# Kernel tuning notes

Hardware: AMD Instinct MI355X
Metric: run time of the kernel (lower is better)

## Reference

```python
import jax, jax.numpy as jnp
import numpy as np

B, C, H, W = 8, 32, 512, 512
BN_EPS = 1e-5


def setup_inputs() -> dict:
    key = jax.random.key(0)
    k1, k2, k3, k4 = jax.random.split(key, 4)
    x = jax.random.normal(k1, (B, C, H, W), dtype=jnp.float32)
    # 1x1 conv weight: [out=4, in=4*C] (kaiming-like scale)
    w_compress = jax.random.normal(k2, (4, 4 * C), dtype=jnp.float32) / np.sqrt(4 * C)
    gamma = jnp.ones((4,), dtype=jnp.float32)
    beta = jnp.zeros((4,), dtype=jnp.float32)
    return {"x": x, "w_compress": w_compress, "gamma": gamma, "beta": beta}


def _four_dir(x):
    # zero-pad H and W by 1; shifted view at (di, dj) gives x[i+di, j+dj]
    xp = jnp.pad(x, ((0, 0), (0, 0), (1, 1), (1, 1)))

    def sh(di, dj):
        return jax.lax.dynamic_slice(xp, (0, 0, 1 + di, 1 + dj), x.shape)

    # PyTorch conv = cross-correlation: kernel one at (r,c) reads x[i+r-1, j+c-1]
    ne = sh(-1, +1) - x
    nw = sh(-1, -1) - x
    se = sh(+1, +1) - x
    sw = sh(+1, -1) - x
    return jnp.concatenate([ne, nw, se, sw], axis=1)  # [B, 4C, H, W]


def reference(x, w_compress, gamma, beta):
    feat = _four_dir(x)
    # 1x1 conv: channel mixing 4C -> 4
    y = jnp.einsum("oc,bchw->bohw", w_compress, feat)
    # BatchNorm2d (training mode: batch statistics, biased variance)
    mean = jnp.mean(y, axis=(0, 2, 3), keepdims=True)
    var = jnp.var(y, axis=(0, 2, 3), keepdims=True)
    y_hat = (y - mean) * jax.lax.rsqrt(var + BN_EPS)
    return y_hat * gamma[None, :, None, None] + beta[None, :, None, None]
```

## Files before the change

### kernel.cpp

```cpp
#include <hip/hip_runtime.h>

#define B_ 8
#define C_ 32
#define H_ 512
#define W_ 512
#define HW_ (H_ * W_)
#define BN_EPS 1e-5f

typedef float f4v __attribute__((ext_vector_type(4)));


__global__ __launch_bounds__(256, 2) void fourdir_compute(
    const float* __restrict__ x,
    const float* __restrict__ w,
    float* __restrict__ y,
    float* __restrict__ sums)
{
    __shared__ f4v wl4[5][C_];
    const int t = threadIdx.x;
    {
        float* wl = (float*)wl4;
        for (int idx = t; idx < 4 * 4 * C_; idx += 256) {
            int o  = idx & 3;
            int dc = idx >> 2;
            wl[idx] = w[o * (4 * C_) + dc];
        }
    }
    __syncthreads();
    if (t < 4 * C_) {
        float* wl = (float*)wl4;
        wl[512 + t] = -(wl[t] + wl[128 + t] + wl[256 + t] + wl[384 + t]);
    }
    __syncthreads();

    const int n    = (int)blockIdx.x;
    const int tile = ((n & 7) << 6) | (n >> 3);
    const int cx   = tile & 1;
    const int iy   = (tile >> 1) & 31;
    const int b    = tile >> 6;

    const int lane = t & 63;
    const int wv   = t >> 6;
    const int c0 = cx << 8;
    const int i0 = (iy << 4) + (wv << 2);
    const int j  = c0 + (lane << 2);
    const float* xb = x + (size_t)b * C_ * HW_;

    const bool jm = (c0 > 0);
    const bool jp = (c0 + 256 < W_);
    const bool tv = (i0 > 0);
    const bool bv = (i0 + 4 < H_);
    const bool edgeL = (lane == 0);
    const bool edgeR = (lane == 63);

    int off[6];
    {
        const int rows[6] = { tv ? i0 - 1 : 0, i0, i0 + 1, i0 + 2, i0 + 3,
                              bv ? i0 + 4 : 0 };
#pragma unroll
        for (int k = 0; k < 6; ++k) off[k] = rows[k] * W_ + j;
    }

    f4v acc[4][4];
#pragma unroll
    for (int p = 0; p < 4; ++p)
#pragma unroll
        for (int q = 0; q < 4; ++q) acc[p][q] = f4v{0.f, 0.f, 0.f, 0.f};

    auto LOADCH = [&](int c, f4v (&vr)[6], float (&le)[6], float (&re)[6]) {
        const float* xc = xb + (size_t)c * HW_;
#pragma unroll
        for (int k = 0; k < 6; ++k) vr[k] = *(const f4v*)(xc + off[k]);
#pragma unroll
        for (int k = 0; k < 6; ++k) {
            float l = 0.f, r = 0.f;
            if (edgeL && jm) l = xc[off[k] - 1];
            if (edgeR && jp) r = xc[off[k] + 4];
            le[k] = l;
            re[k] = r;
        }
        if (!tv) { vr[0] = f4v{0.f,0.f,0.f,0.f}; le[0] = 0.f; re[0] = 0.f; }
        if (!bv) { vr[5] = f4v{0.f,0.f,0.f,0.f}; le[5] = 0.f; re[5] = 0.f; }
    };

    auto COMPCH = [&](int c, const f4v (&vr)[6],
                      const float (&le)[6], const float (&re)[6]) {
        const f4v wne = wl4[0][c];
        const f4v wnw = wl4[1][c];
        const f4v wse = wl4[2][c];
        const f4v wsw = wl4[3][c];
        const f4v wct = wl4[4][c];

        float lf[6], rt[6];
#pragma unroll
        for (int k = 0; k < 6; ++k) {
            const float l = __shfl_up(vr[k][3], 1, 64);
            const float r = __shfl_down(vr[k][0], 1, 64);
            lf[k] = edgeL ? le[k] : l;
            rt[k] = edgeR ? re[k] : r;
        }

#pragma unroll
        for (int p = 0; p < 4; ++p) {
#pragma unroll
            for (int q = 0; q < 4; ++q) {
                const float ne = (q < 3) ? vr[p][q + 1]     : rt[p];
                const float nw = (q > 0) ? vr[p][q - 1]     : lf[p];
                const float se = (q < 3) ? vr[p + 2][q + 1] : rt[p + 2];
                const float sw = (q > 0) ? vr[p + 2][q - 1] : lf[p + 2];
                const float ct = vr[p + 1][q];
                acc[p][q] += wne * ne + wnw * nw + wse * se + wsw * sw + wct * ct;
            }
        }
    };

    f4v vrA[6], vrB[6];
    float leA[6], reA[6], leB[6], reB[6];

    LOADCH(0, vrA, leA, reA);
#pragma unroll 1
    for (int cc = 0; cc < C_ - 2; cc += 2) {
        LOADCH(cc + 1, vrB, leB, reB);
        COMPCH(cc, vrA, leA, reA);
        LOADCH(cc + 2, vrA, leA, reA);
        COMPCH(cc + 1, vrB, leB, reB);
    }
    LOADCH(C_ - 1, vrB, leB, reB);
    COMPCH(C_ - 2, vrA, leA, reA);
    COMPCH(C_ - 1, vrB, leB, reB);

#pragma unroll
    for (int p = 0; p < 4; ++p) {
        const size_t base = (size_t)(i0 + p) * W_ + j;
#pragma unroll
        for (int o = 0; o < 4; ++o) {
            f4v st = { acc[p][0][o], acc[p][1][o], acc[p][2][o], acc[p][3][o] };
            *(f4v*)(y + ((size_t)(b * 4 + o)) * HW_ + base) = st;
        }
    }

    f4v s0 = f4v{0.f,0.f,0.f,0.f}, s1 = f4v{0.f,0.f,0.f,0.f};
#pragma unroll
    for (int p = 0; p < 4; ++p)
#pragma unroll
        for (int q = 0; q < 4; ++q) {
            s0 += acc[p][q];
            s1 += acc[p][q] * acc[p][q];
        }

    float vals[8] = { s0[0], s0[1], s0[2], s0[3], s1[0], s1[1], s1[2], s1[3] };
#pragma unroll
    for (int k = 0; k < 8; ++k) {
        float v = vals[k];
#pragma unroll
        for (int o = 32; o >= 1; o >>= 1) v += __shfl_xor(v, o, 64);
        vals[k] = v;
    }

    __shared__ float red[4][8];
    if (lane == 0) {
#pragma unroll
        for (int k = 0; k < 8; ++k) red[wv][k] = vals[k];
    }
    __syncthreads();
    if (t < 8) {
        const float s = red[0][t] + red[1][t] + red[2][t] + red[3][t];
        atomicAdd(&sums[t], s);
    }
}

__global__ __launch_bounds__(256) void bn_norm(
    float* __restrict__ y,
    const float* __restrict__ sums,
    const float* __restrict__ gamma,
    const float* __restrict__ beta)
{
    const int n = (int)blockIdx.x;
    const int m = ((n & 7) << 8) | (n >> 3);

    const int o = (m >> 6) & 3;

    const float nn = (float)((size_t)B_ * HW_);
    const float mean  = sums[o] / nn;
    const float var   = sums[4 + o] / nn - mean * mean;
    const float scale = rsqrtf(var + BN_EPS) * gamma[o];
    const float shift = beta[o] - mean * scale;

    float* base = y + ((size_t)m * 1024 + threadIdx.x) * 4;
#pragma unroll
    for (int k = 0; k < 4; ++k) {
        f4v v = *(const f4v*)(base + (size_t)k * 256 * 4);
        v = v * scale + shift;
        *(f4v*)(base + (size_t)k * 256 * 4) = v;
    }
}

extern "C" void kernel_launch(void* const* d_in, const int* in_sizes, int n_in,
                              void* d_out, int out_size, void* d_ws, size_t ws_size,
                              hipStream_t stream) {
    const float* x     = (const float*)d_in[0];
    const float* w     = (const float*)d_in[1];
    const float* gamma = (const float*)d_in[2];
    const float* beta  = (const float*)d_in[3];
    float* out  = (float*)d_out;
    float* sums = (float*)d_ws;

    hipMemsetAsync(sums, 0, 8 * sizeof(float), stream);

    fourdir_compute<<<dim3(512), 256, 0, stream>>>(x, w, out, sums);
    bn_norm<<<dim3(2048), 256, 0, stream>>>(out, sums, gamma, beta);
}
```

Measured before the change: 385.8 us.

## Fuse batchnorm into compute kernel via grid-wide barrier on block partials

Merges the normalization pass into the conv kernel. Each block writes its per-channel partial sums, then all blocks wait at an atomic-counter grid barrier, reduce all partials, and apply scale/shift to their register-held results before a single store. This removes the second kernel's full read/write of the output and the atomicAdd contention. It relies on all 512 blocks being co-resident (256 CUs x 2 blocks); otherwise the spin-wait guard times out and the results come out wrong.

```diff
diff --git a/kernel.cpp b/kernel.cpp
--- a/kernel.cpp
+++ b/kernel.cpp
@@ -6,15 +6,19 @@
 #define W_ 512
 #define HW_ (H_ * W_)
 #define BN_EPS 1e-5f
+#define NBLK 512
 
 typedef float f4v __attribute__((ext_vector_type(4)));
 
 
-__global__ __launch_bounds__(256, 2) void fourdir_compute(
+__global__ __launch_bounds__(256, 2) void fourdir_fused(
     const float* __restrict__ x,
     const float* __restrict__ w,
     float* __restrict__ y,
-    float* __restrict__ sums)
+    float* __restrict__ part,
+    unsigned* __restrict__ counter,
+    const float* __restrict__ gamma,
+    const float* __restrict__ beta)
 {
     __shared__ f4v wl4[5][C_];
     const int t = threadIdx.x;
@@ -38,6 +42,7 @@
     const int cx   = tile & 1;
     const int iy   = (tile >> 1) & 31;
     const int b    = tile >> 6;
+    const int bid  = n;
 
     const int lane = t & 63;
     const int wv   = t >> 6;
@@ -129,6 +134,83 @@
     COMPCH(C_ - 2, vrA, leA, reA);
     COMPCH(C_ - 1, vrB, leB, reB);
 
+    f4v s0 = f4v{0.f,0.f,0.f,0.f}, s1 = f4v{0.f,0.f,0.f,0.f};
+#pragma unroll
+    for (int p = 0; p < 4; ++p)
+#pragma unroll
+        for (int q = 0; q < 4; ++q) {
+            s0 += acc[p][q];
+            s1 += acc[p][q] * acc[p][q];
+        }
+
+    float vals[8] = { s0[0], s0[1], s0[2], s0[3], s1[0], s1[1], s1[2], s1[3] };
+#pragma unroll
+    for (int k = 0; k < 8; ++k) {
+        float v = vals[k];
+#pragma unroll
+        for (int o = 32; o >= 1; o >>= 1) v += __shfl_xor(v, o, 64);
+        vals[k] = v;
+    }
+
+    __shared__ float red[4][8];
+    if (lane == 0) {
+#pragma unroll
+        for (int k = 0; k < 8; ++k) red[wv][k] = vals[k];
+    }
+    __syncthreads();
+    if (t < 8) {
+        part[bid * 8 + t] = red[0][t] + red[1][t] + red[2][t] + red[3][t];
+    }
+
+    __threadfence();
+    __syncthreads();
+    if (t == 0) {
+        __hip_atomic_fetch_add(counter, 1u, __ATOMIC_ACQ_REL,
+                               __HIP_MEMORY_SCOPE_AGENT);
+        int guard = 0;
+        while (__hip_atomic_load(counter, __ATOMIC_ACQUIRE,
+                                 __HIP_MEMORY_SCOPE_AGENT) < (unsigned)NBLK &&
+               ++guard < (1 << 21)) {
+            __builtin_amdgcn_s_sleep(8);
+        }
+    }
+    __syncthreads();
+
+    float p8 = 0.f;
+    const int k8 = t & 7;
+#pragma unroll 4
+    for (int ib = (t >> 3); ib < NBLK; ib += 32) p8 += part[ib * 8 + k8];
+
+    __shared__ float redf[256];
+    __shared__ float tot[8];
+    redf[t] = p8;
+    __syncthreads();
+    if (t < 64) {
+        float v = redf[t] + redf[t + 64] + redf[t + 128] + redf[t + 192];
+        v += __shfl_xor(v, 8, 64);
+        v += __shfl_xor(v, 16, 64);
+        v += __shfl_xor(v, 32, 64);
+        if (t < 8) tot[t] = v;
+    }
+    __syncthreads();
+
+    const float nn = (float)((size_t)B_ * HW_);
+    f4v scale, shift;
+#pragma unroll
+    for (int o = 0; o < 4; ++o) {
+        const float mean = tot[o] / nn;
+        const float var  = tot[4 + o] / nn - mean * mean;
+        const float sc   = rsqrtf(var + BN_EPS) * gamma[o];
+        scale[o] = sc;
+        shift[o] = beta[o] - mean * sc;
+    }
+
+#pragma unroll
+    for (int p = 0; p < 4; ++p)
+#pragma unroll
+        for (int q = 0; q < 4; ++q)
+            acc[p][q] = acc[p][q] * scale + shift;
+
 #pragma unroll
     for (int p = 0; p < 4; ++p) {
         const size_t base = (size_t)(i0 + p) * W_ + j;
@@ -137,61 +219,6 @@
             f4v st = { acc[p][0][o], acc[p][1][o], acc[p][2][o], acc[p][3][o] };
             *(f4v*)(y + ((size_t)(b * 4 + o)) * HW_ + base) = st;
         }
-    }
-
-    f4v s0 = f4v{0.f,0.f,0.f,0.f}, s1 = f4v{0.f,0.f,0.f,0.f};
-#pragma unroll
-    for (int p = 0; p < 4; ++p)
-#pragma unroll
-        for (int q = 0; q < 4; ++q) {
-            s0 += acc[p][q];
-            s1 += acc[p][q] * acc[p][q];
-        }
-
-    float vals[8] = { s0[0], s0[1], s0[2], s0[3], s1[0], s1[1], s1[2], s1[3] };
-#pragma unroll
-    for (int k = 0; k < 8; ++k) {
-        float v = vals[k];
-#pragma unroll
-        for (int o = 32; o >= 1; o >>= 1) v += __shfl_xor(v, o, 64);
-        vals[k] = v;
-    }
-
-    __shared__ float red[4][8];
-    if (lane == 0) {
-#pragma unroll
-        for (int k = 0; k < 8; ++k) red[wv][k] = vals[k];
-    }
-    __syncthreads();
-    if (t < 8) {
-        const float s = red[0][t] + red[1][t] + red[2][t] + red[3][t];
-        atomicAdd(&sums[t], s);
-    }
-}
-
-__global__ __launch_bounds__(256) void bn_norm(
-    float* __restrict__ y,
-    const float* __restrict__ sums,
-    const float* __restrict__ gamma,
-    const float* __restrict__ beta)
-{
-    const int n = (int)blockIdx.x;
-    const int m = ((n & 7) << 8) | (n >> 3);
-
-    const int o = (m >> 6) & 3;
-
-    const float nn = (float)((size_t)B_ * HW_);
-    const float mean  = sums[o] / nn;
-    const float var   = sums[4 + o] / nn - mean * mean;
-    const float scale = rsqrtf(var + BN_EPS) * gamma[o];
-    const float shift = beta[o] - mean * scale;
-
-    float* base = y + ((size_t)m * 1024 + threadIdx.x) * 4;
-#pragma unroll
-    for (int k = 0; k < 4; ++k) {
-        f4v v = *(const f4v*)(base + (size_t)k * 256 * 4);
-        v = v * scale + shift;
-        *(f4v*)(base + (size_t)k * 256 * 4) = v;
     }
 }
 
@@ -203,10 +230,11 @@
     const float* gamma = (const float*)d_in[2];
     const float* beta  = (const float*)d_in[3];
     float* out  = (float*)d_out;
-    float* sums = (float*)d_ws;
-
-    hipMemsetAsync(sums, 0, 8 * sizeof(float), stream);
-
-    fourdir_compute<<<dim3(512), 256, 0, stream>>>(x, w, out, sums);
-    bn_norm<<<dim3(2048), 256, 0, stream>>>(out, sums, gamma, beta);
+    float* part = (float*)d_ws;
+    unsigned* counter = (unsigned*)((char*)d_ws + 16384);
+
+    hipMemsetAsync(counter, 0, sizeof(unsigned), stream);
+
+    fourdir_fused<<<dim3(NBLK), 256, 0, stream>>>(x, w, out, part, counter,
+                                                  gamma, beta);
 }
```

Result: slower. 504.4 us (+30.7%).
